# Kernel optimization log

Measured on AMD Instinct MI355X. Metric: run time of the kernel, lower is better.

## Reference

```python
import jax, jax.numpy as jnp
import numpy as np

N_NODES = 1000
HIDDEN = 256
IN_DIM = 128
N_EDGES = 64000


def setup_inputs() -> dict:
    key = jax.random.key(0)
    ks = jax.random.split(key, 24)
    inp = {
        "x": jax.random.normal(ks[0], (N_NODES, IN_DIM), dtype=jnp.float32),
        "edge_index": jax.random.randint(ks[1], (2, N_EDGES), 0, N_NODES, dtype=jnp.int64),
    }
    dims = [(HIDDEN, 2 * IN_DIM)] + [(HIDDEN, 2 * HIDDEN)] * 4
    for l, (dout, din) in enumerate(dims):
        s0 = 1.0 / np.sqrt(din)
        s1 = 1.0 / np.sqrt(HIDDEN)
        inp[f"w{l}_0"] = jax.random.normal(ks[2 + 4 * l], (dout, din), dtype=jnp.float32) * s0
        inp[f"b{l}_0"] = jax.random.normal(ks[3 + 4 * l], (dout,), dtype=jnp.float32) * s0
        inp[f"w{l}_1"] = jax.random.normal(ks[4 + 4 * l], (HIDDEN, HIDDEN), dtype=jnp.float32) * s1
        inp[f"b{l}_1"] = jax.random.normal(ks[5 + 4 * l], (HIDDEN,), dtype=jnp.float32) * s1
    return inp


def _edge_conv(x, src, dst, w1, b1, w2, b2):
    # gather endpoint features per edge: [E, D]
    x_i = x[dst]  # destination (edge_index[1])
    x_j = x[src]  # source (edge_index[0])
    m = jnp.concatenate([x_i, x_j - x_i], axis=-1)  # [E, 2D]
    h = jax.nn.relu(m @ w1.T + b1) @ w2.T + b2      # 2-layer MLP, [E, HIDDEN]
    # scatter-max to destination nodes (include_self=False -> empty rows = 0)
    agg = jax.ops.segment_max(h, dst, num_segments=N_NODES)
    agg = jnp.where(jnp.isneginf(agg), jnp.zeros((), agg.dtype), agg)
    return jax.nn.relu(agg)


def reference(x, edge_index, w0_0, b0_0, w0_1, b0_1, w1_0, b1_0, w1_1, b1_1,
              w2_0, b2_0, w2_1, b2_1, w3_0, b3_0, w3_1, b3_1, w4_0, b4_0, w4_1, b4_1):
    src = edge_index[0]
    dst = edge_index[1]
    params = [(w0_0, b0_0, w0_1, b0_1), (w1_0, b1_0, w1_1, b1_1),
              (w2_0, b2_0, w2_1, b2_1), (w3_0, b3_0, w3_1, b3_1),
              (w4_0, b4_0, w4_1, b4_1)]
    h = x
    for (w1, b1, w2, b2) in params:
        h = _edge_conv(h, src, dst, w1, b1, w2, b2)
    return h
```

## Files before the change

kernel.cpp:

```cpp
#include <hip/hip_runtime.h>

#define NN 1000
#define NE 64000
#define HH 256

typedef _Float16 half8 __attribute__((ext_vector_type(8)));
typedef float floatx4 __attribute__((ext_vector_type(4)));

struct PrepArgs { const float* w0[5]; const float* w1[5]; };


__global__ __launch_bounds__(256) void k_prep(PrepArgs pa,
                                              _Float16* wnode, _Float16* w2h,
                                              int* counts, int* cursor,
                                              float* agg0, float* out) {
    int gtid = blockIdx.x * 256 + threadIdx.x;
    int gstride = gridDim.x * 256;
    for (int i = gtid; i < 1024; i += gstride) { counts[i] = 0; cursor[i] = 0; }
    for (int l = 0; l < 5; l++) {
        const int KK = l ? 8 : 4;
        const int D = KK * 32;
        const int lgKK = l ? 3 : 2;
        const float* w0 = pa.w0[l];
        _Float16* wn = wnode + l * 131072;
        for (int i = gtid; i < 16384 * KK; i += gstride) {
            int j = i & 7;
            int lane = (i >> 3) & 63;
            int nt = (i >> 9) & 1;
            int kk = (i >> 10) & (KK - 1);
            int slice = i >> (10 + lgKK);
            int mn = lane & 15, q = lane >> 4;
            int n = slice * 32 + nt * 16 + mn;
            int k = kk * 32 + q * 8 + j;
            float v = (n < 256) ? (w0[n * 2 * D + k] - w0[n * 2 * D + D + k])
                                : w0[(n - 256) * 2 * D + D + k];
            wn[i] = (_Float16)v;
        }
        const float* w1 = pa.w1[l];
        _Float16* w2 = w2h + l * 65536;
        for (int i = gtid; i < 65536; i += gstride) {
            int j = i & 7;
            int lane = (i >> 3) & 63;
            int nt = (i >> 9) & 3;
            int kk = (i >> 11) & 7;
            int ws = (i >> 14) & 3;
            int mn = lane & 15, q = lane >> 4;
            int row = ws * 64 + nt * 16 + mn;
            int col = kk * 32 + q * 8 + j;
            w2[i] = (_Float16)w1[row * 256 + col];
        }
    }
    floatx4 z = {0.f, 0.f, 0.f, 0.f};
    floatx4* p4 = (floatx4*)agg0;
    for (int i = gtid; i < 4 * NN * HH / 4; i += gstride) p4[i] = z;
    floatx4* o4 = (floatx4*)out;
    for (int i = gtid; i < NN * HH / 4; i += gstride) o4[i] = z;
}

template <int NK>
__device__ __forceinline__ void node_tile(const float* __restrict__ X,
                                          const _Float16* __restrict__ Wn,
                                          const float* __restrict__ b0,
                                          _Float16* __restrict__ out, int bid) {
    const int Kd = NK * 32;
    int t = threadIdx.x;
    int wave = t >> 6, lane = t & 63;
    int q = lane >> 4, mn = lane & 15;
    int m0 = (bid % 63) * 16;
    int n0 = (bid / 63) * 128 + wave * 32;
    int slice = (bid / 63) * 4 + wave;
    int rr = m0 + mn;
    if (rr >= NN) rr = NN - 1;

    half8 afa[NK];
    half8 bfa[NK][2];
#pragma unroll
    for (int kk = 0; kk < NK; kk++) {
        int ka = kk * 32 + q * 8;
        const float* p = X + (size_t)rr * Kd + ka;
        floatx4 x0 = *(const floatx4*)p;
        floatx4 x1 = *(const floatx4*)(p + 4);
        half8 aa;
#pragma unroll
        for (int j = 0; j < 4; j++) { aa[j] = (_Float16)x0[j]; aa[4 + j] = (_Float16)x1[j]; }
        afa[kk] = aa;
        bfa[kk][0] = *(const half8*)(Wn + (((slice * NK + kk) * 2 + 0) * 64 + lane) * 8);
        bfa[kk][1] = *(const half8*)(Wn + (((slice * NK + kk) * 2 + 1) * 64 + lane) * 8);
    }
    floatx4 acc[2] = {};
#pragma unroll
    for (int kk = 0; kk < NK; kk++) {
        acc[0] = __builtin_amdgcn_mfma_f32_16x16x32_f16(afa[kk], bfa[kk][0], acc[0], 0, 0, 0);
        acc[1] = __builtin_amdgcn_mfma_f32_16x16x32_f16(afa[kk], bfa[kk][1], acc[1], 0, 0, 0);
    }
#pragma unroll
    for (int nt = 0; nt < 2; nt++) {
        int col = n0 + nt * 16 + mn;
        float bias = (col < 256) ? b0[col] : 0.f;
#pragma unroll
        for (int r2 = 0; r2 < 4; r2++) {
            int orow = m0 + q * 4 + r2;
            if (orow < NN)
                out[(size_t)orow * 512 + col] = (_Float16)(acc[nt][r2] + bias);
        }
    }
}

__global__ __launch_bounds__(256) void k_hist_node0(const int* __restrict__ ei,
                                                    int* __restrict__ counts,
                                                    const float* __restrict__ X,
                                                    const _Float16* __restrict__ Wn,
                                                    const float* __restrict__ b0,
                                                    _Float16* __restrict__ out) {
    int bid = blockIdx.x;
    if (bid < 4) {
        for (int e = bid * 256 + threadIdx.x; e < NE; e += 4 * 256)
            atomicAdd(&counts[ei[NE + e] & 1023], 1);
    } else {
        node_tile<4>(X, Wn, b0, out, bid - 4);
    }
}

__global__ __launch_bounds__(256) void k_scatter2(const int* __restrict__ ei,
                                                  const int* __restrict__ counts,
                                                  int* __restrict__ cursor,
                                                  int* __restrict__ ssrc,
                                                  int* __restrict__ sdst) {
    __shared__ int sbase[1024];
    __shared__ int ssum[256];
    int t = threadIdx.x;
    int base = t * 4;
    int c4[4]; int sum = 0;
#pragma unroll
    for (int j = 0; j < 4; j++) { c4[j] = counts[base + j]; sum += c4[j]; }
    ssum[t] = sum;
    __syncthreads();
    for (int d = 1; d < 256; d <<= 1) {
        int v = (t >= d) ? ssum[t - d] : 0;
        __syncthreads();
        ssum[t] += v;
        __syncthreads();
    }
    int run = (t > 0) ? ssum[t - 1] : 0;
#pragma unroll
    for (int j = 0; j < 4; j++) { sbase[base + j] = run; run += c4[j]; }
    __syncthreads();
    for (int e = blockIdx.x * 256 + t; e < NE; e += gridDim.x * 256) {
        int s = ei[e] & 1023, d = ei[NE + e] & 1023;
        int pos = sbase[d] + atomicAdd(&cursor[d], 1);
        if (pos < NE) { ssrc[pos] = s; sdst[pos] = d; }
    }
}

__global__ __launch_bounds__(256) void k_node(const float* __restrict__ agg_in,
                                              const _Float16* __restrict__ Wn,
                                              const float* __restrict__ b0,
                                              _Float16* __restrict__ out) {
    node_tile<8>(agg_in, Wn, b0, out, blockIdx.x);
}

__device__ __forceinline__ void edge_mfma(const _Float16* __restrict__ node_ab,
                                          const int* __restrict__ ssrc,
                                          const int* __restrict__ sdst,
                                          const _Float16* __restrict__ W2,
                                          int tile, _Float16* h1, int* sd,
                                          floatx4 acc[4][4]) {
    int t = threadIdx.x;
    int e0 = tile * 64;
    int wave = t >> 6, lane = t & 63;
    int q = lane >> 4, mn = lane & 15;
    const _Float16* W2w = W2 + wave * 16384;

    if (t < 64) sd[t] = sdst[e0 + t];
    {
        int row = t & 63;
        int cb = (t >> 6) * 8;
        int dn = sdst[e0 + row], sn = ssrc[e0 + row];
        const _Float16* pa = node_ab + (size_t)dn * 512 + cb * 8;
        const _Float16* pb = node_ab + (size_t)sn * 512 + 256 + cb * 8;
        half8 av[8], bv[8];
#pragma unroll
        for (int i = 0; i < 8; i++) av[i] = *(const half8*)(pa + i * 8);
#pragma unroll
        for (int i = 0; i < 8; i++) bv[i] = *(const half8*)(pb + i * 8);
#pragma unroll
        for (int i = 0; i < 8; i++) {
            int c = cb + i;
            int p = (c & ~7) | ((c ^ row) & 7);
            half8 hv = av[i] + bv[i];
#pragma unroll
            for (int j = 0; j < 8; j++) hv[j] = hv[j] > (_Float16)0 ? hv[j] : (_Float16)0;
            *(half8*)(&h1[row * 256 + p * 8]) = hv;
        }
    }
    __syncthreads();

#pragma unroll
    for (int kk = 0; kk < 8; kk++) {
        half8 bf[4];
#pragma unroll
        for (int nt = 0; nt < 4; nt++)
            bf[nt] = *(const half8*)(W2w + (kk * 4 + nt) * 512 + lane * 8);
        half8 af[4];
#pragma unroll
        for (int mt = 0; mt < 4; mt++) {
            int r = mt * 16 + mn;
            int c = kk * 4 + q;
            int p = (c & ~7) | ((c ^ r) & 7);
            af[mt] = *(const half8*)(&h1[r * 256 + p * 8]);
        }
#pragma unroll
        for (int mt = 0; mt < 4; mt++)
#pragma unroll
            for (int nt = 0; nt < 4; nt++)
                acc[mt][nt] = __builtin_amdgcn_mfma_f32_16x16x32_f16(af[mt], bf[nt], acc[mt][nt], 0, 0, 0);
    }
}

__global__ __launch_bounds__(256, 4) void edge_gemm2(const _Float16* __restrict__ node_ab,
                          const int* __restrict__ ssrc, const int* __restrict__ sdst,
                          const _Float16* __restrict__ W2, const float* __restrict__ b2,
                          float* __restrict__ agg) {
    __shared__ _Float16 h1[64 * 256];
    __shared__ int sd[64];
    int t = threadIdx.x;
    int wave = t >> 6, lane = t & 63;
    int q = lane >> 4, mn = lane & 15;

    floatx4 acc[4][4] = {};
    edge_mfma(node_ab, ssrc, sdst, W2, blockIdx.x, h1, sd, acc);

    __syncthreads();
#pragma unroll
    for (int nt = 0; nt < 4; nt++) {
        int col = wave * 64 + nt * 16 + mn;
        float bias = b2[col];
        int g = col >> 3, o = col & 7;
#pragma unroll
        for (int mt = 0; mt < 4; mt++) {
#pragma unroll
            for (int r2 = 0; r2 < 4; r2++) {
                int row = mt * 16 + q * 4 + r2;
                float v = acc[mt][nt][r2] + bias;
                v = v > 0.f ? v : 0.f;
                int pg = (g & ~7) | ((g ^ row) & 7);
                h1[row * 256 + pg * 8 + o] = (_Float16)v;
            }
        }
    }
    __syncthreads();

    {
        int c = t;
        int g = c >> 3, o = c & 7;
        float* aggc = agg + c;
        float m = (float)h1[g * 8 + o];
        bool sedge = true;
        int prevd = sd[0];
#pragma unroll 8
        for (int r = 1; r < 64; r++) {
            int d = sd[r];
            int pg = (g & ~7) | ((g ^ r) & 7);
            float v = (float)h1[r * 256 + pg * 8 + o];
            if (d != prevd) {
                if (sedge) {
                    if (m > 0.f)
                        atomicMax((unsigned int*)(aggc + (size_t)prevd * HH), __float_as_uint(m));
                } else {
                    if (m > 0.f)
                        aggc[(size_t)prevd * HH] = m;
                }
                m = v; sedge = false; prevd = d;
            } else {
                m = fmaxf(m, v);
            }
        }
        if (m > 0.f)
            atomicMax((unsigned int*)(aggc + (size_t)prevd * HH), __float_as_uint(m));
    }
}

__global__ __launch_bounds__(256, 4) void edge_last(
        const _Float16* __restrict__ node_ab,
        const int* __restrict__ ssrc, const int* __restrict__ sdst,
        const _Float16* __restrict__ W2, const float* __restrict__ b2,
        float* __restrict__ agg) {
    __shared__ float sf[64 * 129];
    __shared__ int sd[64];
    _Float16* h1 = (_Float16*)sf;
    int t = threadIdx.x;
    int wave = t >> 6, lane = t & 63;
    int q = lane >> 4, mn = lane & 15;

    floatx4 acc[4][4] = {};
    edge_mfma(node_ab, ssrc, sdst, W2, blockIdx.x, h1, sd, acc);

    __syncthreads();
#pragma unroll
    for (int p = 0; p < 2; p++) {
        if (p) __syncthreads();
        if ((wave >> 1) == p) {
            int lc0 = (wave & 1) * 64;
#pragma unroll
            for (int nt = 0; nt < 4; nt++) {
                int col = wave * 64 + nt * 16 + mn;
                float bias = b2[col];
                int lc = lc0 + nt * 16 + mn;
#pragma unroll
                for (int mt = 0; mt < 4; mt++) {
#pragma unroll
                    for (int r2 = 0; r2 < 4; r2++) {
                        int row = mt * 16 + q * 4 + r2;
                        float v = acc[mt][nt][r2] + bias;
                        sf[row * 129 + lc] = v > 0.f ? v : 0.f;
                    }
                }
            }
        }
        __syncthreads();
        if (t < 128) {
            float* aggc = agg + p * 128 + t;
            float m = sf[t];
            bool sedge = true;
            int prevd = sd[0];
#pragma unroll 8
            for (int r = 1; r < 64; r++) {
                int d = sd[r];
                float v = sf[r * 129 + t];
                if (d != prevd) {
                    if (sedge) {
                        if (m > 0.f)
                            atomicMax((unsigned int*)(aggc + (size_t)prevd * HH), __float_as_uint(m));
                    } else {
                        if (m > 0.f)
                            aggc[(size_t)prevd * HH] = m;
                    }
                    m = v; sedge = false; prevd = d;
                } else {
                    m = fmaxf(m, v);
                }
            }
            if (m > 0.f)
                atomicMax((unsigned int*)(aggc + (size_t)prevd * HH), __float_as_uint(m));
        }
    }
}

extern "C" void kernel_launch(void* const* d_in, const int* in_sizes, int n_in,
                              void* d_out, int out_size, void* d_ws, size_t ws_size,
                              hipStream_t stream) {
    const float* x = (const float*)d_in[0];
    const int* ei = (const int*)d_in[1];
    PrepArgs pa;
    const float* b0s[5];
    const float* b1s[5];
    for (int l = 0; l < 5; l++) {
        pa.w0[l] = (const float*)d_in[2 + 4 * l];
        b0s[l] = (const float*)d_in[3 + 4 * l];
        pa.w1[l] = (const float*)d_in[4 + 4 * l];
        b1s[l] = (const float*)d_in[5 + 4 * l];
    }

    int* ssrc = (int*)d_ws;
    int* sdst = ssrc + NE;
    int* counts = sdst + NE;
    int* cursor = counts + 1024;
    _Float16* node_ab = (_Float16*)(cursor + 1024);
    float* agg0 = (float*)(node_ab + 1024 * 512);
    float* agg1 = agg0 + NN * HH;
    float* agg2 = agg1 + NN * HH;
    float* agg3 = agg2 + NN * HH;
    _Float16* wnode = (_Float16*)(agg3 + NN * HH);
    _Float16* w2h = wnode + 5 * 131072;

    hipLaunchKernelGGL(k_prep, dim3(256), dim3(256), 0, stream,
                       pa, wnode, w2h, counts, cursor, agg0, (float*)d_out);
    hipLaunchKernelGGL(k_hist_node0, dim3(256), dim3(256), 0, stream,
                       ei, counts, x, wnode, b0s[0], node_ab);
    hipLaunchKernelGGL(k_scatter2, dim3(NE / 256), dim3(256), 0, stream,
                       ei, counts, cursor, ssrc, sdst);

    float* aggs[4] = {agg0, agg1, agg2, agg3};
    for (int l = 0; l < 4; l++) {
        hipLaunchKernelGGL(edge_gemm2, dim3(NE / 64), dim3(256), 0, stream,
                           node_ab, ssrc, sdst, w2h + (size_t)l * 65536, b1s[l], aggs[l]);
        hipLaunchKernelGGL(k_node, dim3(252), dim3(256), 0, stream,
                           aggs[l], wnode + (size_t)(l + 1) * 131072, b0s[l + 1], node_ab);
    }
    hipLaunchKernelGGL(edge_last, dim3(NE / 64), dim3(256), 0, stream,
                       node_ab, ssrc, sdst, w2h + (size_t)4 * 65536, b1s[4],
                       (float*)d_out);
}
```

Before: 271.9 us.

## Merge prep, histogram and layer-0 node GEMM into one launch

Fuses the weight-prep kernel and the histogram/node0 kernel into a single launch of 524 blocks. The layer-0 node tile now reads fp32 weights directly and converts them in registers, so it no longer waits on prep. The histogram is split into 16 per-block private count arrays, which k_scatter2 sums, to cut atomic contention. This removes one launch and a serial dependency, at the cost of 16x more reads of the counts in every scatter block.

```diff
diff --git a/kernel.cpp b/kernel.cpp
--- a/kernel.cpp
+++ b/kernel.cpp
@@ -9,53 +9,6 @@
 
 struct PrepArgs { const float* w0[5]; const float* w1[5]; };
 
-
-__global__ __launch_bounds__(256) void k_prep(PrepArgs pa,
-                                              _Float16* wnode, _Float16* w2h,
-                                              int* counts, int* cursor,
-                                              float* agg0, float* out) {
-    int gtid = blockIdx.x * 256 + threadIdx.x;
-    int gstride = gridDim.x * 256;
-    for (int i = gtid; i < 1024; i += gstride) { counts[i] = 0; cursor[i] = 0; }
-    for (int l = 0; l < 5; l++) {
-        const int KK = l ? 8 : 4;
-        const int D = KK * 32;
-        const int lgKK = l ? 3 : 2;
-        const float* w0 = pa.w0[l];
-        _Float16* wn = wnode + l * 131072;
-        for (int i = gtid; i < 16384 * KK; i += gstride) {
-            int j = i & 7;
-            int lane = (i >> 3) & 63;
-            int nt = (i >> 9) & 1;
-            int kk = (i >> 10) & (KK - 1);
-            int slice = i >> (10 + lgKK);
-            int mn = lane & 15, q = lane >> 4;
-            int n = slice * 32 + nt * 16 + mn;
-            int k = kk * 32 + q * 8 + j;
-            float v = (n < 256) ? (w0[n * 2 * D + k] - w0[n * 2 * D + D + k])
-                                : w0[(n - 256) * 2 * D + D + k];
-            wn[i] = (_Float16)v;
-        }
-        const float* w1 = pa.w1[l];
-        _Float16* w2 = w2h + l * 65536;
-        for (int i = gtid; i < 65536; i += gstride) {
-            int j = i & 7;
-            int lane = (i >> 3) & 63;
-            int nt = (i >> 9) & 3;
-            int kk = (i >> 11) & 7;
-            int ws = (i >> 14) & 3;
-            int mn = lane & 15, q = lane >> 4;
-            int row = ws * 64 + nt * 16 + mn;
-            int col = kk * 32 + q * 8 + j;
-            w2[i] = (_Float16)w1[row * 256 + col];
-        }
-    }
-    floatx4 z = {0.f, 0.f, 0.f, 0.f};
-    floatx4* p4 = (floatx4*)agg0;
-    for (int i = gtid; i < 4 * NN * HH / 4; i += gstride) p4[i] = z;
-    floatx4* o4 = (floatx4*)out;
-    for (int i = gtid; i < NN * HH / 4; i += gstride) o4[i] = z;
-}
 
 template <int NK>
 __device__ __forceinline__ void node_tile(const float* __restrict__ X,
@@ -106,23 +59,145 @@
     }
 }
 
-__global__ __launch_bounds__(256) void k_hist_node0(const int* __restrict__ ei,
-                                                    int* __restrict__ counts,
-                                                    const float* __restrict__ X,
-                                                    const _Float16* __restrict__ Wn,
-                                                    const float* __restrict__ b0,
-                                                    _Float16* __restrict__ out) {
+__device__ __forceinline__ void node_tile0(const float* __restrict__ X,
+                                           const float* __restrict__ w0,
+                                           const float* __restrict__ b0,
+                                           _Float16* __restrict__ out, int bid) {
+    const int NK = 4;
+    const int Kd = 128;
+    int t = threadIdx.x;
+    int wave = t >> 6, lane = t & 63;
+    int q = lane >> 4, mn = lane & 15;
+    int m0 = (bid % 63) * 16;
+    int n0 = (bid / 63) * 128 + wave * 32;
+    int slice = (bid / 63) * 4 + wave;
+    int rr = m0 + mn;
+    if (rr >= NN) rr = NN - 1;
+
+    half8 afa[NK];
+    half8 bfa[NK][2];
+#pragma unroll
+    for (int kk = 0; kk < NK; kk++) {
+        int ka = kk * 32 + q * 8;
+        const float* p = X + (size_t)rr * Kd + ka;
+        floatx4 x0 = *(const floatx4*)p;
+        floatx4 x1 = *(const floatx4*)(p + 4);
+        half8 aa;
+#pragma unroll
+        for (int j = 0; j < 4; j++) { aa[j] = (_Float16)x0[j]; aa[4 + j] = (_Float16)x1[j]; }
+        afa[kk] = aa;
+#pragma unroll
+        for (int nt = 0; nt < 2; nt++) {
+            int n = slice * 32 + nt * 16 + mn;
+            int k = kk * 32 + q * 8;
+            half8 bb;
+            if (n < 256) {
+                const float* pa = w0 + (size_t)n * 256 + k;
+                floatx4 a0 = *(const floatx4*)pa;
+                floatx4 a1 = *(const floatx4*)(pa + 4);
+                floatx4 c0 = *(const floatx4*)(pa + 128);
+                floatx4 c1 = *(const floatx4*)(pa + 132);
+#pragma unroll
+                for (int j = 0; j < 4; j++) {
+                    bb[j] = (_Float16)(a0[j] - c0[j]);
+                    bb[4 + j] = (_Float16)(a1[j] - c1[j]);
+                }
+            } else {
+                const float* pb = w0 + (size_t)(n - 256) * 256 + 128 + k;
+                floatx4 c0 = *(const floatx4*)pb;
+                floatx4 c1 = *(const floatx4*)(pb + 4);
+#pragma unroll
+                for (int j = 0; j < 4; j++) {
+                    bb[j] = (_Float16)c0[j];
+                    bb[4 + j] = (_Float16)c1[j];
+                }
+            }
+            bfa[kk][nt] = bb;
+        }
+    }
+    floatx4 acc[2] = {};
+#pragma unroll
+    for (int kk = 0; kk < NK; kk++) {
+        acc[0] = __builtin_amdgcn_mfma_f32_16x16x32_f16(afa[kk], bfa[kk][0], acc[0], 0, 0, 0);
+        acc[1] = __builtin_amdgcn_mfma_f32_16x16x32_f16(afa[kk], bfa[kk][1], acc[1], 0, 0, 0);
+    }
+#pragma unroll
+    for (int nt = 0; nt < 2; nt++) {
+        int col = n0 + nt * 16 + mn;
+        float bias = (col < 256) ? b0[col] : 0.f;
+#pragma unroll
+        for (int r2 = 0; r2 < 4; r2++) {
+            int orow = m0 + q * 4 + r2;
+            if (orow < NN)
+                out[(size_t)orow * 512 + col] = (_Float16)(acc[nt][r2] + bias);
+        }
+    }
+}
+
+__global__ __launch_bounds__(256) void k_pre1(PrepArgs pa,
+                                              const int* __restrict__ ei,
+                                              const float* __restrict__ X,
+                                              const float* __restrict__ b0_0,
+                                              _Float16* __restrict__ node_ab,
+                                              _Float16* wnode, _Float16* w2h,
+                                              int* cnts16, int* cursor,
+                                              float* agg0, float* dout) {
     int bid = blockIdx.x;
-    if (bid < 4) {
-        for (int e = bid * 256 + threadIdx.x; e < NE; e += 4 * 256)
-            atomicAdd(&counts[ei[NE + e] & 1023], 1);
+    int t = threadIdx.x;
+    if (bid < 16) {
+        int* my = cnts16 + bid * 1024;
+        for (int i = t; i < 1024; i += 256) my[i] = 0;
+        __syncthreads();
+        for (int e = bid * 256 + t; e < NE; e += 16 * 256)
+            atomicAdd(&my[ei[NE + e] & 1023], 1);
+    } else if (bid < 16 + 252) {
+        node_tile0(X, pa.w0[0], b0_0, node_ab, bid - 16);
     } else {
-        node_tile<4>(X, Wn, b0, out, bid - 4);
+        int gtid = (bid - 268) * 256 + t;
+        int gs = 256 * 256;
+        for (int i = gtid; i < 1024; i += gs) cursor[i] = 0;
+        for (int l = 1; l < 5; l++) {
+            const float* w0 = pa.w0[l];
+            _Float16* wn = wnode + l * 131072;
+            for (int i = gtid; i < 131072; i += gs) {
+                int j = i & 7;
+                int lane = (i >> 3) & 63;
+                int nt = (i >> 9) & 1;
+                int kk = (i >> 10) & 7;
+                int slice = i >> 13;
+                int mn = lane & 15, q = lane >> 4;
+                int n = slice * 32 + nt * 16 + mn;
+                int k = kk * 32 + q * 8 + j;
+                float v = (n < 256) ? (w0[n * 512 + k] - w0[n * 512 + 256 + k])
+                                    : w0[(n - 256) * 512 + 256 + k];
+                wn[i] = (_Float16)v;
+            }
+        }
+        for (int l = 0; l < 5; l++) {
+            const float* w1 = pa.w1[l];
+            _Float16* w2 = w2h + l * 65536;
+            for (int i = gtid; i < 65536; i += gs) {
+                int j = i & 7;
+                int lane = (i >> 3) & 63;
+                int nt = (i >> 9) & 3;
+                int kk = (i >> 11) & 7;
+                int ws = (i >> 14) & 3;
+                int mn = lane & 15, q = lane >> 4;
+                int row = ws * 64 + nt * 16 + mn;
+                int col = kk * 32 + q * 8 + j;
+                w2[i] = (_Float16)w1[row * 256 + col];
+            }
+        }
+        floatx4 z = {0.f, 0.f, 0.f, 0.f};
+        floatx4* p4 = (floatx4*)agg0;
+        for (int i = gtid; i < 4 * NN * HH / 4; i += gs) p4[i] = z;
+        floatx4* o4 = (floatx4*)dout;
+        for (int i = gtid; i < NN * HH / 4; i += gs) o4[i] = z;
     }
 }
 
 __global__ __launch_bounds__(256) void k_scatter2(const int* __restrict__ ei,
-                                                  const int* __restrict__ counts,
+                                                  const int* __restrict__ cnts16,
                                                   int* __restrict__ cursor,
                                                   int* __restrict__ ssrc,
                                                   int* __restrict__ sdst) {
@@ -132,7 +207,12 @@
     int base = t * 4;
     int c4[4]; int sum = 0;
 #pragma unroll
-    for (int j = 0; j < 4; j++) { c4[j] = counts[base + j]; sum += c4[j]; }
+    for (int j = 0; j < 4; j++) {
+        int c = 0;
+#pragma unroll
+        for (int b = 0; b < 16; b++) c += cnts16[b * 1024 + base + j];
+        c4[j] = c; sum += c;
+    }
     ssum[t] = sum;
     __syncthreads();
     for (int d = 1; d < 256; d <<= 1) {
@@ -363,8 +443,8 @@
 
     int* ssrc = (int*)d_ws;
     int* sdst = ssrc + NE;
-    int* counts = sdst + NE;
-    int* cursor = counts + 1024;
+    int* cnts16 = sdst + NE;
+    int* cursor = cnts16 + 16 * 1024;
     _Float16* node_ab = (_Float16*)(cursor + 1024);
     float* agg0 = (float*)(node_ab + 1024 * 512);
     float* agg1 = agg0 + NN * HH;
@@ -373,12 +453,11 @@
     _Float16* wnode = (_Float16*)(agg3 + NN * HH);
     _Float16* w2h = wnode + 5 * 131072;
 
-    hipLaunchKernelGGL(k_prep, dim3(256), dim3(256), 0, stream,
-                       pa, wnode, w2h, counts, cursor, agg0, (float*)d_out);
-    hipLaunchKernelGGL(k_hist_node0, dim3(256), dim3(256), 0, stream,
-                       ei, counts, x, wnode, b0s[0], node_ab);
+    hipLaunchKernelGGL(k_pre1, dim3(524), dim3(256), 0, stream,
+                       pa, ei, x, b0s[0], node_ab, wnode, w2h,
+                       cnts16, cursor, agg0, (float*)d_out);
     hipLaunchKernelGGL(k_scatter2, dim3(NE / 256), dim3(256), 0, stream,
-                       ei, counts, cursor, ssrc, sdst);
+                       ei, cnts16, cursor, ssrc, sdst);
 
     float* aggs[4] = {agg0, agg1, agg2, agg3};
     for (int l = 0; l < 4; l++) {
```

After: 252.9 us. -7.0%, faster.
